# Performance work log

Hardware: AMD Instinct MI355X
Metric: run time of the kernel (lower is better)

The kernel has to match this reference:

```python
import jax, jax.numpy as jnp
import numpy as np

B = 128           # persons in batch
V = 128           # visits per person
CPV = 16          # codes per visit
MAX_VISITS = 510  # 512 - 2, hard-coded in module
D = 256           # embedding_dim * n_heads = 128 * 2
H = 2             # n_heads
DH = D // H
MAX_DAYS = 365
VOCAB = 30000
N_LAYERS = 2
DFF = 4 * D


def setup_inputs() -> dict:
    key = jax.random.key(0)
    ks = jax.random.split(key, 24)
    total_visits = B * V
    total_codes = total_visits * CPV
    all_codes = jax.random.randint(ks[0], (total_codes,), 0, VOCAB, dtype=jnp.int32)
    # code -> visit segment id (contiguous, as produced by the per-person loop)
    seg_ids = (jnp.arange(total_codes, dtype=jnp.int32) // CPV).astype(jnp.int32)
    # visit -> flattened slot in padded [B, MAX_VISITS] tensor (right-aligned)
    pos = MAX_VISITS - V + jnp.arange(V, dtype=jnp.int32)
    dest = (jnp.arange(B, dtype=jnp.int32)[:, None] * MAX_VISITS + pos[None, :]).reshape(-1)
    times = jax.random.uniform(ks[1], (total_visits,), minval=0.0, maxval=float(MAX_DAYS), dtype=jnp.float32)
    s = 0.02
    concept_emb = jax.random.normal(ks[2], (VOCAB, D), dtype=jnp.float32) * s
    pad_emb = jnp.zeros((D,), dtype=jnp.float32)
    Wq = jax.random.normal(ks[3], (N_LAYERS, D, D), dtype=jnp.float32) * s
    Wk = jax.random.normal(ks[4], (N_LAYERS, D, D), dtype=jnp.float32) * s
    Wv = jax.random.normal(ks[5], (N_LAYERS, D, D), dtype=jnp.float32) * s
    Wo = jax.random.normal(ks[6], (N_LAYERS, D, D), dtype=jnp.float32) * s
    W1 = jax.random.normal(ks[7], (N_LAYERS, D, DFF), dtype=jnp.float32) * s
    W2 = jax.random.normal(ks[8], (N_LAYERS, DFF, D), dtype=jnp.float32) * s
    z = lambda *sh: jnp.zeros(sh, dtype=jnp.float32)
    o = lambda *sh: jnp.ones(sh, dtype=jnp.float32)
    return dict(all_codes=all_codes, seg_ids=seg_ids, dest=dest, times=times,
                concept_emb=concept_emb, pad_emb=pad_emb,
                Wq=Wq, Wk=Wk, Wv=Wv, Wo=Wo,
                bq=z(N_LAYERS, D), bk=z(N_LAYERS, D), bv=z(N_LAYERS, D), bo=z(N_LAYERS, D),
                ln1_g=o(N_LAYERS, D), ln1_b=z(N_LAYERS, D),
                W1=W1, b1=z(N_LAYERS, DFF), W2=W2, b2=z(N_LAYERS, D),
                ln2_g=o(N_LAYERS, D), ln2_b=z(N_LAYERS, D))


def _ln(x, g, b):
    m = jnp.mean(x, axis=-1, keepdims=True)
    v = jnp.var(x, axis=-1, keepdims=True)
    return g * (x - m) * jax.lax.rsqrt(v + 1e-5) + b


def _forward(all_codes, seg_ids, dest, times, concept_emb, pad_emb,
             Wq, Wk, Wv, Wo, bq, bk, bv, bo, ln1_g, ln1_b,
             W1, b1, W2, b2, ln2_g, ln2_b):
    # gather code embeddings and segment-sum per visit (index_add_ in torch)
    emb = concept_emb[all_codes]                               # [total_codes, D]
    summed = jax.ops.segment_sum(emb, seg_ids, num_segments=B * V)  # [B*V, D]
    # scatter visits right-aligned into padded [B*MAX_VISITS, D], pad slots = pad_emb
    padded = jnp.broadcast_to(pad_emb, (B * MAX_VISITS, D)).at[dest].set(summed)
    # sinusoidal time embedding: timescales = ((1/1e4)**(1/D))**arange(D/2)
    t = jnp.clip(times, 0.0, float(MAX_DAYS - 1))
    ts = jnp.power(jnp.float32((1.0 / 10000.0) ** (1.0 / D)), jnp.arange(D // 2, dtype=jnp.float32))
    ang = t[:, None] * ts[None, :]                             # [B*V, D/2]
    te = jnp.concatenate([jnp.sin(ang), jnp.cos(ang)], axis=1) # [B*V, D]
    te_pad = jnp.zeros((B * MAX_VISITS, D), dtype=padded.dtype).at[dest].set(te)
    x = (padded + te_pad).reshape(B, MAX_VISITS, D)
    inv_sqrt_dh = np.float32(1.0 / np.sqrt(DH))
    for l in range(N_LAYERS):
        q = (x @ Wq[l] + bq[l]).reshape(B, MAX_VISITS, H, DH)
        k = (x @ Wk[l] + bk[l]).reshape(B, MAX_VISITS, H, DH)
        v = (x @ Wv[l] + bv[l]).reshape(B, MAX_VISITS, H, DH)
        scores = jnp.einsum('bqhd,bkhd->bhqk', q, k) * inv_sqrt_dh
        attn = jax.nn.softmax(scores, axis=-1)
        ctx = jnp.einsum('bhqk,bkhd->bqhd', attn, v).reshape(B, MAX_VISITS, D)
        x = _ln(x + ctx @ Wo[l] + bo[l], ln1_g[l], ln1_b[l])
        ff = jax.nn.relu(x @ W1[l] + b1[l]) @ W2[l] + b2[l]
        x = _ln(x + ff, ln2_g[l], ln2_b[l])
    return x


def reference(all_codes, seg_ids, dest, times, concept_emb, pad_emb,
              Wq, Wk, Wv, Wo, bq, bk, bv, bo, ln1_g, ln1_b,
              W1, b1, W2, b2, ln2_g, ln2_b):
    return _forward(all_codes, seg_ids, dest, times, concept_emb, pad_emb,
                    Wq, Wk, Wv, Wo, bq, bk, bv, bo, ln1_g, ln1_b,
                    W1, b1, W2, b2, ln2_g, ln2_b)
```

## Files before the change

### kernel.cpp

```cpp
#include <hip/hip_runtime.h>
#include <cstddef>

#define BATCH 128
#define NV 128
#define CPV 16
#define MAXV 510
#define SC 256
#define NPAD 382
#define DIM 256
#define NH 2
#define DH 128
#define NLAYERS 2
#define DFF 1024
#define MROWS (BATCH * SC)

typedef __attribute__((ext_vector_type(8))) short short8;
typedef __attribute__((ext_vector_type(4))) short short4v;
typedef __attribute__((ext_vector_type(4))) float floatx4;

__device__ __forceinline__ short f2bf(float f) {
    union { float f; unsigned u; } v; v.f = f;
    unsigned r = v.u + 0x7fffu + ((v.u >> 16) & 1u);
    return (short)(r >> 16);
}
__device__ __forceinline__ float bf2f(short s) {
    union { unsigned u; float f; } v; v.u = ((unsigned)(unsigned short)s) << 16;
    return v.f;
}

__device__ __forceinline__ void gload_lds16(const short* g, short* l) {
    __builtin_amdgcn_global_load_lds(
        (const __attribute__((address_space(1))) unsigned int*)g,
        (__attribute__((address_space(3))) unsigned int*)l,
        16, 0, 0);
}

__global__ __launch_bounds__(256) void wtrans_all(const float* __restrict__ Wq,
                                                  const float* __restrict__ Wk,
                                                  const float* __restrict__ Wv,
                                                  const float* __restrict__ Wo,
                                                  const float* __restrict__ W1,
                                                  const float* __restrict__ W2,
                                                  short* __restrict__ wqkvT,
                                                  short* __restrict__ woT,
                                                  short* __restrict__ w1T,
                                                  short* __restrict__ w2T) {
    int y = blockIdx.y;
    int l = y / 6, w = y - l * 6;
    const float* src; short* dst; int K, nsh;
    switch (w) {
        case 0:  src = Wq + (size_t)l * 65536;  dst = wqkvT + (size_t)l * 196608;           K = 256;  nsh = 8;  break;
        case 1:  src = Wk + (size_t)l * 65536;  dst = wqkvT + (size_t)l * 196608 + 65536;   K = 256;  nsh = 8;  break;
        case 2:  src = Wv + (size_t)l * 65536;  dst = wqkvT + (size_t)l * 196608 + 131072;  K = 256;  nsh = 8;  break;
        case 3:  src = Wo + (size_t)l * 65536;  dst = woT   + (size_t)l * 65536;            K = 256;  nsh = 8;  break;
        case 4:  src = W1 + (size_t)l * 262144; dst = w1T   + (size_t)l * 262144;           K = 256;  nsh = 10; break;
        default: src = W2 + (size_t)l * 262144; dst = w2T   + (size_t)l * 262144;           K = 1024; nsh = 8;  break;
    }
    int N = 1 << nsh;
    int idx = blockIdx.x * 256 + threadIdx.x;
    if (idx >= K * N) return;
    int k = idx >> nsh, n = idx & (N - 1);
    dst[(size_t)n * K + k] = f2bf(src[idx]);
}

__global__ __launch_bounds__(256) void build_x(const int* __restrict__ codes,
                                               const float* __restrict__ times,
                                               const float* __restrict__ cemb,
                                               const float* __restrict__ pemb,
                                               short* __restrict__ x) {
    int row = blockIdx.x;
    int d = threadIdx.x;
    int b = row >> 8;
    int r = row & (SC - 1);
    float val;
    if (r > 128) {
        val = 0.f;
    } else if (r == 128) {
        val = pemb[d];
    } else {
        int visit = b * NV + r;
        const int* cb = codes + visit * CPV;
        float s = 0.f;
#pragma unroll
        for (int c = 0; c < CPV; ++c)
            s += cemb[(size_t)cb[c] * DIM + d];
        float t = times[visit];
        t = fminf(fmaxf(t, 0.f), 364.f);
        int i = d & 127;
        float ang = t * expf(-0.03597789207803197f * (float)i);
        float te = (d < 128) ? sinf(ang) : cosf(ang);
        val = s + te;
    }
    x[(size_t)row * DIM + d] = f2bf(val);
}

__global__ __launch_bounds__(256) void gemm_qkv(const short* __restrict__ A,
                                                const short* __restrict__ BT,
                                                const float* __restrict__ bq,
                                                const float* __restrict__ bk,
                                                const float* __restrict__ bv,
                                                short* __restrict__ qo,
                                                short* __restrict__ ko,
                                                short* __restrict__ vo) {
    __shared__ __align__(16) short lA[2][128 * 32];
    __shared__ __align__(16) short lB[2][128 * 32];
    int tid = threadIdx.x;
    int wave = tid >> 6, lane = tid & 63;
    int l15 = lane & 15, quad = lane >> 4;
    int q8 = quad * 8;
    int m0 = blockIdx.y * 128;
    int n0 = blockIdx.x * 128;
    int sel = blockIdx.x >> 1;
    int nloc = n0 & 255;
    int wm = (wave & 1) * 64;
    int wn = (wave >> 1) * 64;

    int srow = tid >> 2;
    int skoff = (tid & 3) * 8;
    const short* ag = A + (size_t)(m0 + srow) * DIM + skoff;
    const short* bg = BT + (size_t)(n0 + srow) * DIM + skoff;
    const size_t rstep = (size_t)64 * DIM;
    int t8 = tid * 8;

    floatx4 acc[4][4];
#pragma unroll
    for (int i = 0; i < 4; ++i)
#pragma unroll
        for (int j = 0; j < 4; ++j) acc[i][j] = (floatx4){0.f, 0.f, 0.f, 0.f};

    gload_lds16(ag, lA[0] + t8);
    gload_lds16(ag + rstep, lA[0] + 2048 + t8);
    gload_lds16(bg, lB[0] + t8);
    gload_lds16(bg + rstep, lB[0] + 2048 + t8);
    __syncthreads();
    int cur = 0;
#pragma unroll
    for (int k0 = 0; k0 < 8; ++k0) {
        if (k0 < 7) {
            int kn = (k0 + 1) * 32;
            gload_lds16(ag + kn, lA[cur ^ 1] + t8);
            gload_lds16(ag + rstep + kn, lA[cur ^ 1] + 2048 + t8);
            gload_lds16(bg + kn, lB[cur ^ 1] + t8);
            gload_lds16(bg + rstep + kn, lB[cur ^ 1] + 2048 + t8);
        }
        short8 aF[4], bF[4];
#pragma unroll
        for (int t = 0; t < 4; ++t) {
            aF[t] = *(const short8*)(lA[cur] + (wm + t * 16 + l15) * 32 + q8);
            bF[t] = *(const short8*)(lB[cur] + (wn + t * 16 + l15) * 32 + q8);
        }
#pragma unroll
        for (int i = 0; i < 4; ++i)
#pragma unroll
            for (int j = 0; j < 4; ++j)
                acc[i][j] = __builtin_amdgcn_mfma_f32_16x16x32_bf16(aF[i], bF[j], acc[i][j], 0, 0, 0);
        __syncthreads();
        cur ^= 1;
    }

    const float* bias = (sel == 0) ? bq : (sel == 1) ? bk : bv;
    short* out = (sel == 0) ? qo : (sel == 1) ? ko : vo;
#pragma unroll
    for (int j = 0; j < 4; ++j) {
        int col = nloc + wn + j * 16 + l15;
        float bval = bias[col];
#pragma unroll
        for (int i = 0; i < 4; ++i) {
#pragma unroll
            for (int r = 0; r < 4; ++r) {
                int row = m0 + wm + i * 16 + quad * 4 + r;
                out[(size_t)row * DIM + col] = f2bf(acc[i][j][r] + bval);
            }
        }
    }
}

__global__ __launch_bounds__(256) void gemm_wo_ln(const short* __restrict__ CTX,
                                                  const short* __restrict__ WoT,
                                                  const float* __restrict__ bo,
                                                  const short* __restrict__ X,
                                                  const float* __restrict__ g,
                                                  const float* __restrict__ bta,
                                                  short* __restrict__ xout) {
    __shared__ __align__(16) short lA[2][64 * 32];
    __shared__ __align__(16) short lB[2][256 * 32];
    int tid = threadIdx.x;
    int wave = tid >> 6, lane = tid & 63;
    int l15 = lane & 15, quad = lane >> 4;
    int q8 = quad * 8;
    int m0 = blockIdx.x * 64;
    int wr = wave * 16;
    int srow = tid >> 2;
    int skoff = (tid & 3) * 8;
    const short* ag = CTX + (size_t)(m0 + srow) * DIM + skoff;
    const short* bg = WoT + (size_t)srow * DIM + skoff;
    int t8 = tid * 8;

    floatx4 acc[16];
#pragma unroll
    for (int j = 0; j < 16; ++j) acc[j] = (floatx4){0.f, 0.f, 0.f, 0.f};

    gload_lds16(ag, lA[0] + t8);
    gload_lds16(bg, lB[0] + t8);
    gload_lds16(bg + (size_t)64 * DIM, lB[0] + 2048 + t8);
    gload_lds16(bg + (size_t)128 * DIM, lB[0] + 4096 + t8);
    gload_lds16(bg + (size_t)192 * DIM, lB[0] + 6144 + t8);
    __syncthreads();
    int cur = 0;
#pragma unroll
    for (int k0 = 0; k0 < 8; ++k0) {
        if (k0 < 7) {
            int kn = (k0 + 1) * 32;
            gload_lds16(ag + kn, lA[cur ^ 1] + t8);
            gload_lds16(bg + kn, lB[cur ^ 1] + t8);
            gload_lds16(bg + (size_t)64 * DIM + kn, lB[cur ^ 1] + 2048 + t8);
            gload_lds16(bg + (size_t)128 * DIM + kn, lB[cur ^ 1] + 4096 + t8);
            gload_lds16(bg + (size_t)192 * DIM + kn, lB[cur ^ 1] + 6144 + t8);
        }
        short8 aF = *(const short8*)(lA[cur] + (wr + l15) * 32 + q8);
#pragma unroll
        for (int j = 0; j < 16; ++j) {
            short8 bF = *(const short8*)(lB[cur] + (j * 16 + l15) * 32 + q8);
            acc[j] = __builtin_amdgcn_mfma_f32_16x16x32_bf16(aF, bF, acc[j], 0, 0, 0);
        }
        __syncthreads();
        cur ^= 1;
    }

    float bias[16], gam[16], bet[16];
#pragma unroll
    for (int j = 0; j < 16; ++j) {
        int col = j * 16 + l15;
        bias[j] = bo[col]; gam[j] = g[col]; bet[j] = bta[col];
    }
#pragma unroll
    for (int r = 0; r < 4; ++r) {
        int row = m0 + wr + quad * 4 + r;
        float v[16], s = 0.f, sq = 0.f;
#pragma unroll
        for (int j = 0; j < 16; ++j) {
            v[j] = acc[j][r] + bias[j] + bf2f(X[(size_t)row * DIM + j * 16 + l15]);
            s += v[j]; sq += v[j] * v[j];
        }
        s += __shfl_xor(s, 1); sq += __shfl_xor(sq, 1);
        s += __shfl_xor(s, 2); sq += __shfl_xor(sq, 2);
        s += __shfl_xor(s, 4); sq += __shfl_xor(sq, 4);
        s += __shfl_xor(s, 8); sq += __shfl_xor(sq, 8);
        float mean = s * (1.f / 256.f);
        float var = fmaxf(sq * (1.f / 256.f) - mean * mean, 0.f);
        float rstd = rsqrtf(var + 1e-5f);
#pragma unroll
        for (int j = 0; j < 16; ++j) {
            float y = gam[j] * (v[j] - mean) * rstd + bet[j];
            xout[(size_t)row * DIM + j * 16 + l15] = f2bf(y);
        }
    }
}

#define PST 136
__global__ __launch_bounds__(256, 2) void ff_fused(const short* __restrict__ X,
                                                   const short* __restrict__ W1T,
                                                   const float* __restrict__ b1,
                                                   const short* __restrict__ W2T,
                                                   const float* __restrict__ b2,
                                                   const float* __restrict__ g2,
                                                   const float* __restrict__ bt2,
                                                   short* __restrict__ xout,
                                                   float* __restrict__ fout,
                                                   float* __restrict__ padrow) {
    __shared__ __align__(16) short lA[2][64 * 32];
    __shared__ __align__(16) short lB[2][128 * 32];
    __shared__ __align__(16) short lB2[2][256 * 32];
    __shared__ __align__(16) short lP[64 * PST];
    __shared__ float redS[4][32], redQ[4][32];
    int tid = threadIdx.x;
    int wave = tid >> 6, lane = tid & 63;
    int l15 = lane & 15, quad = lane >> 4;
    int q8 = quad * 8;
    int m0 = blockIdx.x * 64;
    int wm = (wave & 1) * 32;
    int wf = (wave >> 1) * 64;
    int wn2 = (wave >> 1) * 128;
    int srow = tid >> 2;
    int spart = (tid & 3) * 8;
    const short* xg = X + (size_t)(m0 + srow) * DIM + spart;
    int t8 = tid * 8;

    floatx4 acc2[2][8];
#pragma unroll
    for (int i = 0; i < 2; ++i)
#pragma unroll
        for (int j = 0; j < 8; ++j) acc2[i][j] = (floatx4){0.f, 0.f, 0.f, 0.f};

    for (int f0 = 0; f0 < DFF; f0 += 128) {
        const short* w1g = W1T + (size_t)(f0 + srow) * DIM + spart;
        floatx4 acc1[2][4];
#pragma unroll
        for (int i = 0; i < 2; ++i)
#pragma unroll
            for (int j = 0; j < 4; ++j) acc1[i][j] = (floatx4){0.f, 0.f, 0.f, 0.f};

        gload_lds16(xg, lA[0] + t8);
        gload_lds16(w1g, lB[0] + t8);
        gload_lds16(w1g + (size_t)64 * DIM, lB[0] + 2048 + t8);
        __syncthreads();
        int cur = 0;
#pragma unroll
        for (int k0 = 0; k0 < 8; ++k0) {
            if (k0 < 7) {
                int kn = (k0 + 1) * 32;
                gload_lds16(xg + kn, lA[cur ^ 1] + t8);
                gload_lds16(w1g + kn, lB[cur ^ 1] + t8);
                gload_lds16(w1g + (size_t)64 * DIM + kn, lB[cur ^ 1] + 2048 + t8);
            }
            short8 aF[2], bF[4];
#pragma unroll
            for (int t = 0; t < 2; ++t)
                aF[t] = *(const short8*)(lA[cur] + (wm + t * 16 + l15) * 32 + q8);
#pragma unroll
            for (int t = 0; t < 4; ++t)
                bF[t] = *(const short8*)(lB[cur] + (wf + t * 16 + l15) * 32 + q8);
#pragma unroll
            for (int i = 0; i < 2; ++i)
#pragma unroll
                for (int j = 0; j < 4; ++j)
                    acc1[i][j] = __builtin_amdgcn_mfma_f32_16x16x32_bf16(aF[i], bF[j], acc1[i][j], 0, 0, 0);
            __syncthreads();
            cur ^= 1;
        }

        {
            const short* w2g = W2T + (size_t)srow * DFF + f0 + spart;
            gload_lds16(w2g, lB2[0] + t8);
            gload_lds16(w2g + (size_t)64 * DFF, lB2[0] + 2048 + t8);
            gload_lds16(w2g + (size_t)128 * DFF, lB2[0] + 4096 + t8);
            gload_lds16(w2g + (size_t)192 * DFF, lB2[0] + 6144 + t8);
        }
#pragma unroll
        for (int j = 0; j < 4; ++j) {
            int fc = wf + j * 16 + l15;
            float bval = b1[f0 + fc];
#pragma unroll
            for (int i = 0; i < 2; ++i) {
#pragma unroll
                for (int r = 0; r < 4; ++r) {
                    float v = acc1[i][j][r] + bval;
                    lP[(wm + i * 16 + quad * 4 + r) * PST + fc] = f2bf(fmaxf(v, 0.f));
                }
            }
        }
        __syncthreads();
        cur = 0;
#pragma unroll
        for (int ks = 0; ks < 4; ++ks) {
            if (ks < 3) {
                const short* w2g = W2T + (size_t)srow * DFF + f0 + (ks + 1) * 32 + spart;
                gload_lds16(w2g, lB2[cur ^ 1] + t8);
                gload_lds16(w2g + (size_t)64 * DFF, lB2[cur ^ 1] + 2048 + t8);
                gload_lds16(w2g + (size_t)128 * DFF, lB2[cur ^ 1] + 4096 + t8);
                gload_lds16(w2g + (size_t)192 * DFF, lB2[cur ^ 1] + 6144 + t8);
            }
            short8 aP[2], bW[8];
#pragma unroll
            for (int t = 0; t < 2; ++t)
                aP[t] = *(const short8*)(lP + (wm + t * 16 + l15) * PST + ks * 32 + q8);
#pragma unroll
            for (int j = 0; j < 8; ++j)
                bW[j] = *(const short8*)(lB2[cur] + (wn2 + j * 16 + l15) * 32 + q8);
#pragma unroll
            for (int i = 0; i < 2; ++i)
#pragma unroll
                for (int j = 0; j < 8; ++j)
                    acc2[i][j] = __builtin_amdgcn_mfma_f32_16x16x32_bf16(aP[i], bW[j], acc2[i][j], 0, 0, 0);
            __syncthreads();
            cur ^= 1;
        }
    }

    float b2v[8];
#pragma unroll
    for (int j = 0; j < 8; ++j) b2v[j] = b2[wn2 + j * 16 + l15];
#pragma unroll
    for (int i = 0; i < 2; ++i) {
#pragma unroll
        for (int r = 0; r < 4; ++r) {
            int row = m0 + wm + i * 16 + quad * 4 + r;
            float s = 0.f, sq = 0.f;
#pragma unroll
            for (int j = 0; j < 8; ++j) {
                float v = acc2[i][j][r] + b2v[j] + bf2f(X[(size_t)row * DIM + wn2 + j * 16 + l15]);
                acc2[i][j][r] = v;
                s += v; sq += v * v;
            }
            s += __shfl_xor(s, 1); sq += __shfl_xor(sq, 1);
            s += __shfl_xor(s, 2); sq += __shfl_xor(sq, 2);
            s += __shfl_xor(s, 4); sq += __shfl_xor(sq, 4);
            s += __shfl_xor(s, 8); sq += __shfl_xor(sq, 8);
            if (l15 == 0) {
                int idx = i * 16 + quad * 4 + r;
                redS[wave][idx] = s;
                redQ[wave][idx] = sq;
            }
        }
    }
    __syncthreads();
    float gam[8], bet[8];
#pragma unroll
    for (int j = 0; j < 8; ++j) {
        int col = wn2 + j * 16 + l15;
        gam[j] = g2[col]; bet[j] = bt2[col];
    }
#pragma unroll
    for (int i = 0; i < 2; ++i) {
#pragma unroll
        for (int r = 0; r < 4; ++r) {
            int idx = i * 16 + quad * 4 + r;
            float ts = redS[wave][idx] + redS[wave ^ 2][idx];
            float tq = redQ[wave][idx] + redQ[wave ^ 2][idx];
            float mean = ts * (1.f / 256.f);
            float var = fmaxf(tq * (1.f / 256.f) - mean * mean, 0.f);
            float rstd = rsqrtf(var + 1e-5f);
            int grow = m0 + wm + i * 16 + quad * 4 + r;
            if (!fout) {
#pragma unroll
                for (int j = 0; j < 8; ++j) {
                    float y = gam[j] * (acc2[i][j][r] - mean) * rstd + bet[j];
                    xout[(size_t)grow * DIM + wn2 + j * 16 + l15] = f2bf(y);
                }
            } else {
                int b = grow >> 8, rr = grow & 255;
                if (rr < 128) {
                    float* dst = fout + ((size_t)b * MAXV + NPAD + rr) * DIM;
#pragma unroll
                    for (int j = 0; j < 8; ++j) {
                        float y = gam[j] * (acc2[i][j][r] - mean) * rstd + bet[j];
                        dst[wn2 + j * 16 + l15] = y;
                    }
                } else if (rr == 128) {
#pragma unroll
                    for (int j = 0; j < 8; ++j) {
                        float y = gam[j] * (acc2[i][j][r] - mean) * rstd + bet[j];
                        padrow[(size_t)b * DIM + wn2 + j * 16 + l15] = y;
                    }
                }
            }
        }
    }
}

__global__ __launch_bounds__(256) void pad_bcast(const float* __restrict__ padrow,
                                                 float* __restrict__ fout) {
    int b = blockIdx.y;
    int p = blockIdx.x * 4 + (threadIdx.x >> 6);
    if (p >= NPAD) return;
    int d4 = (threadIdx.x & 63) * 4;
    floatx4 v = *(const floatx4*)(padrow + (size_t)b * DIM + d4);
    *(floatx4*)(fout + ((size_t)b * MAXV + p) * DIM + d4) = v;
}

__global__ __launch_bounds__(256) void transpose_v(const short* __restrict__ v,
                                                   short* __restrict__ vT) {
    __shared__ short lds[32][33];
    int pair = blockIdx.y;
    int b = pair >> 1, h = pair & 1;
    int st = (blockIdx.x & 7) * 32;
    int dt = (blockIdx.x >> 3) * 32;
    int tid = threadIdx.x;
    int sl = tid >> 3, dl = (tid & 7) * 4;
    const short* src = v + ((size_t)(b * SC + st + sl)) * DIM + h * DH + dt + dl;
    short4v val = *(const short4v*)src;
#pragma unroll
    for (int j = 0; j < 4; ++j) lds[sl][dl + j] = val[j];
    __syncthreads();
    int drow = tid >> 3, scol = (tid & 7) * 4;
    short* dst = vT + (size_t)pair * DH * SC + (size_t)(dt + drow) * SC + st + scol;
#pragma unroll
    for (int j = 0; j < 4; ++j) dst[j] = lds[scol + j][drow];
}

#define AST 136
__global__ __launch_bounds__(256) void attn_fused(const short* __restrict__ q,
                                                  const short* __restrict__ k,
                                                  const short* __restrict__ vT,
                                                  short* __restrict__ ctx) {
    __shared__ __align__(16) short lA[128 * 32];
    __shared__ __align__(16) short lB[128 * 32];
    __shared__ __align__(16) short lS[128 * AST];
    int tid = threadIdx.x;
    int wave = tid >> 6, lane = tid & 63;
    int l15 = lane & 15, quad = lane >> 4;
    int q8 = quad * 8;
    int pair = blockIdx.y;
    int b = pair >> 1, h = pair & 1;
    int m0 = blockIdx.x * 128;
    int wm = (wave & 1) * 64;
    int wn = (wave >> 1) * 64;

    const short* Qb = q + ((size_t)b * SC) * DIM + h * DH;
    const short* Kb = k + ((size_t)b * SC) * DIM + h * DH;
    const short* Vb = vT + (size_t)pair * DH * SC;
    int srow = tid >> 2;
    int skoff = (tid & 3) * 8;
    short* lA_dst = lA + tid * 8;
    short* lB_dst = lB + tid * 8;
    const size_t rstep = (size_t)64 * DIM;
    const short* ag = Qb + (size_t)(m0 + srow) * DIM + skoff;
    const float scale = 0.08838834764831845f;

    floatx4 oacc[4][4];
#pragma unroll
    for (int i = 0; i < 4; ++i)
#pragma unroll
        for (int j = 0; j < 4; ++j) oacc[i][j] = (floatx4){0.f, 0.f, 0.f, 0.f};
    float rsum[4] = {0.f, 0.f, 0.f, 0.f};

    for (int kt = 0; kt < 2; ++kt) {
        const short* bg = Kb + (size_t)(kt * 128 + srow) * DIM + skoff;
        floatx4 sacc[4][4];
#pragma unroll
        for (int i = 0; i < 4; ++i)
#pragma unroll
            for (int j = 0; j < 4; ++j) sacc[i][j] = (floatx4){0.f, 0.f, 0.f, 0.f};
#pragma unroll
        for (int k0 = 0; k0 < DH; k0 += 32) {
            gload_lds16(ag + k0, lA_dst);
            gload_lds16(ag + rstep + k0, lA_dst + 2048);
            gload_lds16(bg + k0, lB_dst);
            gload_lds16(bg + rstep + k0, lB_dst + 2048);
            __syncthreads();
            short8 aF[4], bF[4];
#pragma unroll
            for (int t = 0; t < 4; ++t) {
                aF[t] = *(const short8*)(lA + (wm + t * 16 + l15) * 32 + q8);
                bF[t] = *(const short8*)(lB + (wn + t * 16 + l15) * 32 + q8);
            }
#pragma unroll
            for (int i = 0; i < 4; ++i)
#pragma unroll
                for (int j = 0; j < 4; ++j)
                    sacc[i][j] = __builtin_amdgcn_mfma_f32_16x16x32_bf16(aF[i], bF[j], sacc[i][j], 0, 0, 0);
            __syncthreads();
        }
#pragma unroll
        for (int j = 0; j < 4; ++j) {
            int col = wn + j * 16 + l15;
            int cg = kt * 128 + col;
            float w = (cg < 128) ? 1.f : ((cg == 128) ? (float)NPAD : 0.f);
#pragma unroll
            for (int i = 0; i < 4; ++i) {
#pragma unroll
                for (int r = 0; r < 4; ++r) {
                    float e = __expf(fminf(sacc[i][j][r] * scale, 30.f));
                    lS[(wm + i * 16 + quad * 4 + r) * AST + col] = f2bf(w * e);
                }
            }
        }
        __syncthreads();
#pragma unroll
        for (int ks = 0; ks < 4; ++ks) {
            const short* vg = Vb + (size_t)srow * SC + kt * 128 + ks * 32 + skoff;
            gload_lds16(vg, lB_dst);
            gload_lds16(vg + (size_t)64 * SC, lB_dst + 2048);
            __syncthreads();
            short8 aP[4], bV[4];
#pragma unroll
            for (int t = 0; t < 4; ++t) {
                aP[t] = *(const short8*)(lS + (wm + t * 16 + l15) * AST + ks * 32 + q8);
                bV[t] = *(const short8*)(lB + (wn + t * 16 + l15) * 32 + q8);
            }
#pragma unroll
            for (int i = 0; i < 4; ++i) {
                float s = 0.f;
#pragma unroll
                for (int e = 0; e < 8; ++e) s += bf2f(aP[i][e]);
                rsum[i] += s;
            }
#pragma unroll
            for (int i = 0; i < 4; ++i)
#pragma unroll
                for (int j = 0; j < 4; ++j)
                    oacc[i][j] = __builtin_amdgcn_mfma_f32_16x16x32_bf16(aP[i], bV[j], oacc[i][j], 0, 0, 0);
            __syncthreads();
        }
    }

#pragma unroll
    for (int i = 0; i < 4; ++i) {
        rsum[i] += __shfl_xor(rsum[i], 16);
        rsum[i] += __shfl_xor(rsum[i], 32);
    }
    short* outb = ctx + ((size_t)(b * SC + m0)) * DIM + h * DH;
#pragma unroll
    for (int i = 0; i < 4; ++i) {
#pragma unroll
        for (int r = 0; r < 4; ++r) {
            float inv = 1.f / __shfl(rsum[i], quad * 4 + r);
#pragma unroll
            for (int j = 0; j < 4; ++j) {
                int col = wn + j * 16 + l15;
                int row = wm + i * 16 + quad * 4 + r;
                outb[(size_t)row * DIM + col] = f2bf(oacc[i][j][r] * inv);
            }
        }
    }
}

extern "C" void kernel_launch(void* const* d_in, const int* in_sizes, int n_in,
                              void* d_out, int out_size, void* d_ws, size_t ws_size,
                              hipStream_t stream) {
    const int*   all_codes = (const int*)d_in[0];
    const float* times = (const float*)d_in[3];
    const float* cemb  = (const float*)d_in[4];
    const float* pemb  = (const float*)d_in[5];
    const float* Wq = (const float*)d_in[6];
    const float* Wk = (const float*)d_in[7];
    const float* Wv = (const float*)d_in[8];
    const float* Wo = (const float*)d_in[9];
    const float* bq = (const float*)d_in[10];
    const float* bk = (const float*)d_in[11];
    const float* bv = (const float*)d_in[12];
    const float* bo = (const float*)d_in[13];
    const float* ln1g = (const float*)d_in[14];
    const float* ln1b = (const float*)d_in[15];
    const float* W1 = (const float*)d_in[16];
    const float* b1 = (const float*)d_in[17];
    const float* W2 = (const float*)d_in[18];
    const float* b2 = (const float*)d_in[19];
    const float* ln2g = (const float*)d_in[20];
    const float* ln2b = (const float*)d_in[21];

    char* ws = (char*)d_ws;
    short* wqkvT = (short*)ws;
    short* woT   = wqkvT + 2 * 196608;
    short* w1T   = woT + 2 * 65536;
    short* w2T   = w1T + 2 * 262144;
    float* padrow = (float*)(ws + (3500u << 10));

    const size_t SLOT = (size_t)MROWS * DIM;
    short* xb = (short*)(ws + (4u << 20));
    short* C0 = xb + SLOT;
    short* C1 = C0 + SLOT;
    short* C2 = C1 + SLOT;
    short* C3 = C2 + SLOT;
    short* C4 = C3 + SLOT;

    wtrans_all<<<dim3(1024, 12), 256, 0, stream>>>(Wq, Wk, Wv, Wo, W1, W2,
                                                   wqkvT, woT, w1T, w2T);
    build_x<<<MROWS, 256, 0, stream>>>(all_codes, times, cemb, pemb, xb);

    for (int l = 0; l < NLAYERS; ++l) {
        const short* qkv_l = wqkvT + (size_t)l * 196608;
        const short* wo_l = woT + (size_t)l * 65536;
        const short* w1_l = w1T + (size_t)l * 262144;
        const short* w2_l = w2T + (size_t)l * 262144;
        int last = (l == NLAYERS - 1);

        gemm_qkv<<<dim3(6, MROWS / 128), 256, 0, stream>>>(xb, qkv_l, bq + l * 256, bk + l * 256,
                                                           bv + l * 256, C0, C1, C2);
        transpose_v<<<dim3(32, BATCH * NH), 256, 0, stream>>>(C2, C4);
        attn_fused<<<dim3(2, BATCH * NH), 256, 0, stream>>>(C0, C1, C4, C3);
        gemm_wo_ln<<<MROWS / 64, 256, 0, stream>>>(C3, wo_l, bo + l * 256, xb,
                                                   ln1g + l * 256, ln1b + l * 256, C0);
        ff_fused<<<MROWS / 64, 256, 0, stream>>>(C0, w1_l, b1 + l * 1024, w2_l, b2 + l * 256,
                                                 ln2g + l * 256, ln2b + l * 256, xb,
                                                 last ? (float*)d_out : nullptr,
                                                 last ? padrow : nullptr);
        if (last)
            pad_bcast<<<dim3(96, BATCH), 256, 0, stream>>>(padrow, (float*)d_out);
    }
}
```

Measured before the change: 458.7 us.

## Drop padded rows from main GEMMs and handle the pad row separately

Shrinks the per-person sequence from 256 slots (128 real visits, one pad representative, zero rows) to exactly 128 real rows. This halves the rows in the QKV, Wo and FFN GEMMs and in attention. The single shared pad row is computed by small per-batch kernels: pad_qkv projects it, and pad_tail runs its attention, Wo+LN and FFN+LN with scalar dot products. Attention appends the pad key as an extra column weighted by 382, with V transposed to a 160 stride. This adds extra launches and slow scalar per-row kernels in exchange for halving the bulk work.

```diff
diff --git a/kernel.cpp b/kernel.cpp
--- a/kernel.cpp
+++ b/kernel.cpp
@@ -5,14 +5,15 @@
 #define NV 128
 #define CPV 16
 #define MAXV 510
-#define SC 256
 #define NPAD 382
 #define DIM 256
 #define NH 2
 #define DH 128
 #define NLAYERS 2
 #define DFF 1024
-#define MROWS (BATCH * SC)
+#define MROWS (BATCH * NV)
+#define AST 168
+#define VST 160
 
 typedef __attribute__((ext_vector_type(8))) short short8;
 typedef __attribute__((ext_vector_type(4))) short short4v;
@@ -66,32 +67,28 @@
 __global__ __launch_bounds__(256) void build_x(const int* __restrict__ codes,
                                                const float* __restrict__ times,
                                                const float* __restrict__ cemb,
-                                               const float* __restrict__ pemb,
                                                short* __restrict__ x) {
     int row = blockIdx.x;
     int d = threadIdx.x;
-    int b = row >> 8;
-    int r = row & (SC - 1);
-    float val;
-    if (r > 128) {
-        val = 0.f;
-    } else if (r == 128) {
-        val = pemb[d];
-    } else {
-        int visit = b * NV + r;
-        const int* cb = codes + visit * CPV;
-        float s = 0.f;
-#pragma unroll
-        for (int c = 0; c < CPV; ++c)
-            s += cemb[(size_t)cb[c] * DIM + d];
-        float t = times[visit];
-        t = fminf(fmaxf(t, 0.f), 364.f);
-        int i = d & 127;
-        float ang = t * expf(-0.03597789207803197f * (float)i);
-        float te = (d < 128) ? sinf(ang) : cosf(ang);
-        val = s + te;
-    }
-    x[(size_t)row * DIM + d] = f2bf(val);
+    int b = row >> 7;
+    int r = row & 127;
+    int visit = b * NV + r;
+    const int* cb = codes + visit * CPV;
+    float s = 0.f;
+#pragma unroll
+    for (int c = 0; c < CPV; ++c)
+        s += cemb[(size_t)cb[c] * DIM + d];
+    float t = times[visit];
+    t = fminf(fmaxf(t, 0.f), 364.f);
+    int i = d & 127;
+    float ang = t * expf(-0.03597789207803197f * (float)i);
+    float te = (d < 128) ? sinf(ang) : cosf(ang);
+    x[(size_t)row * DIM + d] = f2bf(s + te);
+}
+
+__global__ __launch_bounds__(256) void build_xpad(const float* __restrict__ pemb,
+                                                  short* __restrict__ xpad) {
+    xpad[(size_t)blockIdx.x * DIM + threadIdx.x] = f2bf(pemb[threadIdx.x]);
 }
 
 __global__ __launch_bounds__(256) void gemm_qkv(const short* __restrict__ A,
@@ -175,6 +172,30 @@
     }
 }
 
+__global__ __launch_bounds__(256) void pad_qkv(const short* __restrict__ xpad,
+                                               const short* __restrict__ qkvT,
+                                               const float* __restrict__ bq,
+                                               const float* __restrict__ bk,
+                                               const float* __restrict__ bv,
+                                               float* __restrict__ padQ,
+                                               short* __restrict__ padK,
+                                               short* __restrict__ padV) {
+    __shared__ float x[256];
+    int b = blockIdx.x, tid = threadIdx.x;
+    x[tid] = bf2f(xpad[(size_t)b * DIM + tid]);
+    __syncthreads();
+#pragma unroll
+    for (int w = 0; w < 3; ++w) {
+        const short* wr = qkvT + (size_t)w * 65536 + (size_t)tid * 256;
+        float a = 0.f;
+#pragma unroll 8
+        for (int k = 0; k < 256; ++k) a += x[k] * bf2f(wr[k]);
+        if (w == 0)      padQ[(size_t)b * DIM + tid] = a + bq[tid];
+        else if (w == 1) padK[(size_t)b * DIM + tid] = f2bf(a + bk[tid]);
+        else             padV[(size_t)b * DIM + tid] = f2bf(a + bv[tid]);
+    }
+}
+
 __global__ __launch_bounds__(256) void gemm_wo_ln(const short* __restrict__ CTX,
                                                   const short* __restrict__ WoT,
                                                   const float* __restrict__ bo,
@@ -266,8 +287,7 @@
                                                    const float* __restrict__ g2,
                                                    const float* __restrict__ bt2,
                                                    short* __restrict__ xout,
-                                                   float* __restrict__ fout,
-                                                   float* __restrict__ padrow) {
+                                                   float* __restrict__ fout) {
     __shared__ __align__(16) short lA[2][64 * 32];
     __shared__ __align__(16) short lB[2][128 * 32];
     __shared__ __align__(16) short lB2[2][256 * 32];
@@ -428,23 +448,127 @@
                     xout[(size_t)grow * DIM + wn2 + j * 16 + l15] = f2bf(y);
                 }
             } else {
-                int b = grow >> 8, rr = grow & 255;
-                if (rr < 128) {
-                    float* dst = fout + ((size_t)b * MAXV + NPAD + rr) * DIM;
-#pragma unroll
-                    for (int j = 0; j < 8; ++j) {
-                        float y = gam[j] * (acc2[i][j][r] - mean) * rstd + bet[j];
-                        dst[wn2 + j * 16 + l15] = y;
-                    }
-                } else if (rr == 128) {
-#pragma unroll
-                    for (int j = 0; j < 8; ++j) {
-                        float y = gam[j] * (acc2[i][j][r] - mean) * rstd + bet[j];
-                        padrow[(size_t)b * DIM + wn2 + j * 16 + l15] = y;
-                    }
+                int bb = grow >> 7, rr = grow & 127;
+                float* dst = fout + ((size_t)bb * MAXV + NPAD + rr) * DIM;
+#pragma unroll
+                for (int j = 0; j < 8; ++j) {
+                    float y = gam[j] * (acc2[i][j][r] - mean) * rstd + bet[j];
+                    dst[wn2 + j * 16 + l15] = y;
                 }
             }
         }
+    }
+}
+
+__global__ __launch_bounds__(256) void pad_tail(const float* __restrict__ padQ,
+                                                const short* __restrict__ padK,
+                                                const short* __restrict__ padV,
+                                                const short* __restrict__ kmain,
+                                                const short* __restrict__ vmain,
+                                                const short* __restrict__ woT,
+                                                const float* __restrict__ bo,
+                                                const float* __restrict__ g1,
+                                                const float* __restrict__ bt1,
+                                                const short* __restrict__ w1T,
+                                                const float* __restrict__ b1,
+                                                const short* __restrict__ w2T,
+                                                const float* __restrict__ b2,
+                                                const float* __restrict__ g2,
+                                                const float* __restrict__ bt2,
+                                                short* __restrict__ xpad,
+                                                float* __restrict__ padrowF) {
+    __shared__ float qv[256], wgt[2][128], wp[2], den[2], ctx[256], h1[256], ff[1024];
+    __shared__ float red[4][2];
+    int b = blockIdx.x, tid = threadIdx.x;
+    int wave = tid >> 6, lane = tid & 63;
+    const float scale = 0.08838834764831845f;
+
+    qv[tid] = padQ[(size_t)b * DIM + tid];
+    __syncthreads();
+    int h = tid >> 7, kk = tid & 127;
+    {
+        const short* krow = kmain + (size_t)(b * NV + kk) * DIM + h * DH;
+        float s = 0.f;
+#pragma unroll 8
+        for (int d = 0; d < DH; ++d) s += bf2f(krow[d]) * qv[h * DH + d];
+        wgt[h][kk] = __expf(fminf(s * scale, 30.f));
+    }
+    if (kk == 0) {
+        const short* kp = padK + (size_t)b * DIM + h * DH;
+        float sp = 0.f;
+#pragma unroll 8
+        for (int d = 0; d < DH; ++d) sp += bf2f(kp[d]) * qv[h * DH + d];
+        wp[h] = 382.f * __expf(fminf(sp * scale, 30.f));
+    }
+    __syncthreads();
+    if (kk == 0) {
+        float dsum = wp[h];
+        for (int i = 0; i < 128; ++i) dsum += wgt[h][i];
+        den[h] = dsum;
+    }
+    __syncthreads();
+    {
+        const short* vcol = vmain + (size_t)(b * NV) * DIM + h * DH + kk;
+        float c = 0.f;
+#pragma unroll 8
+        for (int key = 0; key < 128; ++key) c += wgt[h][key] * bf2f(vcol[(size_t)key * DIM]);
+        c += wp[h] * bf2f(padV[(size_t)b * DIM + h * DH + kk]);
+        ctx[h * DH + kk] = c / den[h];
+    }
+    __syncthreads();
+    float t;
+    {
+        const short* wr = woT + (size_t)tid * 256;
+        float a = 0.f;
+#pragma unroll 8
+        for (int k = 0; k < 256; ++k) a += ctx[k] * bf2f(wr[k]);
+        t = a + bo[tid] + bf2f(xpad[(size_t)b * DIM + tid]);
+    }
+    {
+        float s = t, sq = t * t;
+#pragma unroll
+        for (int off = 1; off < 64; off <<= 1) { s += __shfl_xor(s, off); sq += __shfl_xor(sq, off); }
+        if (lane == 0) { red[wave][0] = s; red[wave][1] = sq; }
+        __syncthreads();
+        float ts = red[0][0] + red[1][0] + red[2][0] + red[3][0];
+        float tq = red[0][1] + red[1][1] + red[2][1] + red[3][1];
+        float mean = ts * (1.f / 256.f);
+        float var = fmaxf(tq * (1.f / 256.f) - mean * mean, 0.f);
+        float rstd = rsqrtf(var + 1e-5f);
+        h1[tid] = g1[tid] * (t - mean) * rstd + bt1[tid];
+    }
+    __syncthreads();
+#pragma unroll
+    for (int u = 0; u < 4; ++u) {
+        int f = u * 256 + tid;
+        const short* wr = w1T + (size_t)f * 256;
+        float a = 0.f;
+#pragma unroll 8
+        for (int k = 0; k < 256; ++k) a += h1[k] * bf2f(wr[k]);
+        ff[f] = fmaxf(a + b1[f], 0.f);
+    }
+    __syncthreads();
+    {
+        const short* wr = w2T + (size_t)tid * DFF;
+        float a = 0.f;
+#pragma unroll 8
+        for (int f = 0; f < DFF; ++f) a += ff[f] * bf2f(wr[f]);
+        t = a + b2[tid] + h1[tid];
+    }
+    {
+        float s = t, sq = t * t;
+#pragma unroll
+        for (int off = 1; off < 64; off <<= 1) { s += __shfl_xor(s, off); sq += __shfl_xor(sq, off); }
+        if (lane == 0) { red[wave][0] = s; red[wave][1] = sq; }
+        __syncthreads();
+        float ts = red[0][0] + red[1][0] + red[2][0] + red[3][0];
+        float tq = red[0][1] + red[1][1] + red[2][1] + red[3][1];
+        float mean = ts * (1.f / 256.f);
+        float var = fmaxf(tq * (1.f / 256.f) - mean * mean, 0.f);
+        float rstd = rsqrtf(var + 1e-5f);
+        float y = g2[tid] * (t - mean) * rstd + bt2[tid];
+        xpad[(size_t)b * DIM + tid] = f2bf(y);
+        if (padrowF) padrowF[(size_t)b * DIM + tid] = y;
     }
 }
 
@@ -459,139 +583,167 @@
 }
 
 __global__ __launch_bounds__(256) void transpose_v(const short* __restrict__ v,
+                                                   const short* __restrict__ padV,
                                                    short* __restrict__ vT) {
     __shared__ short lds[32][33];
     int pair = blockIdx.y;
     int b = pair >> 1, h = pair & 1;
-    int st = (blockIdx.x & 7) * 32;
-    int dt = (blockIdx.x >> 3) * 32;
+    int st = blockIdx.x % 5;
+    int dt = blockIdx.x / 5;
     int tid = threadIdx.x;
     int sl = tid >> 3, dl = (tid & 7) * 4;
-    const short* src = v + ((size_t)(b * SC + st + sl)) * DIM + h * DH + dt + dl;
-    short4v val = *(const short4v*)src;
+    short4v val;
+    if (st < 4) {
+        const short* src = v + ((size_t)(b * NV + st * 32 + sl)) * DIM + h * DH + dt * 32 + dl;
+        val = *(const short4v*)src;
+    } else {
+        val = (short4v){0, 0, 0, 0};
+        if (sl == 0)
+            val = *(const short4v*)(padV + (size_t)b * DIM + h * DH + dt * 32 + dl);
+    }
 #pragma unroll
     for (int j = 0; j < 4; ++j) lds[sl][dl + j] = val[j];
     __syncthreads();
     int drow = tid >> 3, scol = (tid & 7) * 4;
-    short* dst = vT + (size_t)pair * DH * SC + (size_t)(dt + drow) * SC + st + scol;
+    short* dst = vT + (size_t)pair * DH * VST + (size_t)(dt * 32 + drow) * VST + st * 32 + scol;
 #pragma unroll
     for (int j = 0; j < 4; ++j) dst[j] = lds[scol + j][drow];
 }
 
-#define AST 136
 __global__ __launch_bounds__(256) void attn_fused(const short* __restrict__ q,
                                                   const short* __restrict__ k,
                                                   const short* __restrict__ vT,
+                                                  const short* __restrict__ padK,
                                                   short* __restrict__ ctx) {
-    __shared__ __align__(16) short lA[128 * 32];
+    __shared__ __align__(16) short lA[64 * 32];
     __shared__ __align__(16) short lB[128 * 32];
-    __shared__ __align__(16) short lS[128 * AST];
+    __shared__ __align__(16) short lS[64 * AST];
     int tid = threadIdx.x;
     int wave = tid >> 6, lane = tid & 63;
     int l15 = lane & 15, quad = lane >> 4;
     int q8 = quad * 8;
     int pair = blockIdx.y;
     int b = pair >> 1, h = pair & 1;
-    int m0 = blockIdx.x * 128;
-    int wm = (wave & 1) * 64;
+    int m0 = blockIdx.x * 64;
+    int wm = (wave & 1) * 32;
     int wn = (wave >> 1) * 64;
 
-    const short* Qb = q + ((size_t)b * SC) * DIM + h * DH;
-    const short* Kb = k + ((size_t)b * SC) * DIM + h * DH;
-    const short* Vb = vT + (size_t)pair * DH * SC;
     int srow = tid >> 2;
     int skoff = (tid & 3) * 8;
+    const short* ag = q + (size_t)(b * NV + m0 + srow) * DIM + h * DH + skoff;
+    const short* bg = k + (size_t)(b * NV + srow) * DIM + h * DH + skoff;
+    const short* kp = padK + (size_t)b * DIM + h * DH + q8;
     short* lA_dst = lA + tid * 8;
     short* lB_dst = lB + tid * 8;
-    const size_t rstep = (size_t)64 * DIM;
-    const short* ag = Qb + (size_t)(m0 + srow) * DIM + skoff;
     const float scale = 0.08838834764831845f;
 
-    floatx4 oacc[4][4];
-#pragma unroll
-    for (int i = 0; i < 4; ++i)
+    {
+        int zr = tid >> 2, zc = 144 + (tid & 3) * 4;
+        *(short4v*)(lS + zr * AST + zc) = (short4v){0, 0, 0, 0};
+    }
+
+    floatx4 sacc[2][4];
+    floatx4 sacct[2];
+#pragma unroll
+    for (int i = 0; i < 2; ++i) {
+#pragma unroll
+        for (int j = 0; j < 4; ++j) sacc[i][j] = (floatx4){0.f, 0.f, 0.f, 0.f};
+        sacct[i] = (floatx4){0.f, 0.f, 0.f, 0.f};
+    }
+
+#pragma unroll
+    for (int k0 = 0; k0 < DH; k0 += 32) {
+        gload_lds16(ag + k0, lA_dst);
+        gload_lds16(bg + k0, lB_dst);
+        gload_lds16(bg + (size_t)64 * DIM + k0, lB_dst + 2048);
+        __syncthreads();
+        short8 aF[2], bF[4];
+#pragma unroll
+        for (int t = 0; t < 2; ++t)
+            aF[t] = *(const short8*)(lA + (wm + t * 16 + l15) * 32 + q8);
+#pragma unroll
+        for (int t = 0; t < 4; ++t)
+            bF[t] = *(const short8*)(lB + (wn + t * 16 + l15) * 32 + q8);
+#pragma unroll
+        for (int i = 0; i < 2; ++i)
+#pragma unroll
+            for (int j = 0; j < 4; ++j)
+                sacc[i][j] = __builtin_amdgcn_mfma_f32_16x16x32_bf16(aF[i], bF[j], sacc[i][j], 0, 0, 0);
+        if (wn == 0) {
+            short8 bFt = (l15 == 0) ? *(const short8*)(kp + k0) : (short8){0,0,0,0,0,0,0,0};
+#pragma unroll
+            for (int i = 0; i < 2; ++i)
+                sacct[i] = __builtin_amdgcn_mfma_f32_16x16x32_bf16(aF[i], bFt, sacct[i], 0, 0, 0);
+        }
+        __syncthreads();
+    }
+#pragma unroll
+    for (int j = 0; j < 4; ++j) {
+        int col = wn + j * 16 + l15;
+#pragma unroll
+        for (int i = 0; i < 2; ++i) {
+#pragma unroll
+            for (int r = 0; r < 4; ++r) {
+                lS[(wm + i * 16 + quad * 4 + r) * AST + col] =
+                    f2bf(__expf(fminf(sacc[i][j][r] * scale, 30.f)));
+            }
+        }
+    }
+    if (wn == 0) {
+        float wt = (l15 == 0) ? 382.f : 0.f;
+#pragma unroll
+        for (int i = 0; i < 2; ++i) {
+#pragma unroll
+            for (int r = 0; r < 4; ++r) {
+                lS[(wm + i * 16 + quad * 4 + r) * AST + 128 + l15] =
+                    f2bf(wt * __expf(fminf(sacct[i][r] * scale, 30.f)));
+            }
+        }
+    }
+    __syncthreads();
+    const short* vg = vT + (size_t)pair * DH * VST + (size_t)srow * VST + skoff;
+    floatx4 oacc[2][4];
+#pragma unroll
+    for (int i = 0; i < 2; ++i)
 #pragma unroll
         for (int j = 0; j < 4; ++j) oacc[i][j] = (floatx4){0.f, 0.f, 0.f, 0.f};
-    float rsum[4] = {0.f, 0.f, 0.f, 0.f};
-
-    for (int kt = 0; kt < 2; ++kt) {
-        const short* bg = Kb + (size_t)(kt * 128 + srow) * DIM + skoff;
-        floatx4 sacc[4][4];
-#pragma unroll
-        for (int i = 0; i < 4; ++i)
-#pragma unroll
-            for (int j = 0; j < 4; ++j) sacc[i][j] = (floatx4){0.f, 0.f, 0.f, 0.f};
-#pragma unroll
-        for (int k0 = 0; k0 < DH; k0 += 32) {
-            gload_lds16(ag + k0, lA_dst);
-            gload_lds16(ag + rstep + k0, lA_dst + 2048);
-            gload_lds16(bg + k0, lB_dst);
-            gload_lds16(bg + rstep + k0, lB_dst + 2048);
-            __syncthreads();
-            short8 aF[4], bF[4];
-#pragma unroll
-            for (int t = 0; t < 4; ++t) {
-                aF[t] = *(const short8*)(lA + (wm + t * 16 + l15) * 32 + q8);
-                bF[t] = *(const short8*)(lB + (wn + t * 16 + l15) * 32 + q8);
-            }
-#pragma unroll
-            for (int i = 0; i < 4; ++i)
-#pragma unroll
-                for (int j = 0; j < 4; ++j)
-                    sacc[i][j] = __builtin_amdgcn_mfma_f32_16x16x32_bf16(aF[i], bF[j], sacc[i][j], 0, 0, 0);
-            __syncthreads();
-        }
-#pragma unroll
-        for (int j = 0; j < 4; ++j) {
-            int col = wn + j * 16 + l15;
-            int cg = kt * 128 + col;
-            float w = (cg < 128) ? 1.f : ((cg == 128) ? (float)NPAD : 0.f);
-#pragma unroll
-            for (int i = 0; i < 4; ++i) {
-#pragma unroll
-                for (int r = 0; r < 4; ++r) {
-                    float e = __expf(fminf(sacc[i][j][r] * scale, 30.f));
-                    lS[(wm + i * 16 + quad * 4 + r) * AST + col] = f2bf(w * e);
-                }
-            }
-        }
-        __syncthreads();
-#pragma unroll
-        for (int ks = 0; ks < 4; ++ks) {
-            const short* vg = Vb + (size_t)srow * SC + kt * 128 + ks * 32 + skoff;
-            gload_lds16(vg, lB_dst);
-            gload_lds16(vg + (size_t)64 * SC, lB_dst + 2048);
-            __syncthreads();
-            short8 aP[4], bV[4];
-#pragma unroll
-            for (int t = 0; t < 4; ++t) {
-                aP[t] = *(const short8*)(lS + (wm + t * 16 + l15) * AST + ks * 32 + q8);
-                bV[t] = *(const short8*)(lB + (wn + t * 16 + l15) * 32 + q8);
-            }
-#pragma unroll
-            for (int i = 0; i < 4; ++i) {
-                float s = 0.f;
-#pragma unroll
-                for (int e = 0; e < 8; ++e) s += bf2f(aP[i][e]);
-                rsum[i] += s;
-            }
-#pragma unroll
-            for (int i = 0; i < 4; ++i)
-#pragma unroll
-                for (int j = 0; j < 4; ++j)
-                    oacc[i][j] = __builtin_amdgcn_mfma_f32_16x16x32_bf16(aP[i], bV[j], oacc[i][j], 0, 0, 0);
-            __syncthreads();
-        }
-    }
-
-#pragma unroll
-    for (int i = 0; i < 4; ++i) {
+    float rsum[2] = {0.f, 0.f};
+
+#pragma unroll
+    for (int ks = 0; ks < 5; ++ks) {
+        gload_lds16(vg + ks * 32, lB_dst);
+        gload_lds16(vg + (size_t)64 * VST + ks * 32, lB_dst + 2048);
+        __syncthreads();
+        short8 aP[2], bV[4];
+#pragma unroll
+        for (int t = 0; t < 2; ++t)
+            aP[t] = *(const short8*)(lS + (wm + t * 16 + l15) * AST + ks * 32 + q8);
+#pragma unroll
+        for (int t = 0; t < 4; ++t)
+            bV[t] = *(const short8*)(lB + (wn + t * 16 + l15) * 32 + q8);
+#pragma unroll
+        for (int i = 0; i < 2; ++i) {
+            float s = 0.f;
+#pragma unroll
+            for (int e = 0; e < 8; ++e) s += bf2f(aP[i][e]);
+            rsum[i] += s;
+        }
+#pragma unroll
+        for (int i = 0; i < 2; ++i)
+#pragma unroll
+            for (int j = 0; j < 4; ++j)
+                oacc[i][j] = __builtin_amdgcn_mfma_f32_16x16x32_bf16(aP[i], bV[j], oacc[i][j], 0, 0, 0);
+        __syncthreads();
+    }
+
+#pragma unroll
+    for (int i = 0; i < 2; ++i) {
         rsum[i] += __shfl_xor(rsum[i], 16);
         rsum[i] += __shfl_xor(rsum[i], 32);
     }
-    short* outb = ctx + ((size_t)(b * SC + m0)) * DIM + h * DH;
-#pragma unroll
-    for (int i = 0; i < 4; ++i) {
+    short* outb = ctx + (size_t)(b * NV + m0) * DIM + h * DH;
+#pragma unroll
+    for (int i = 0; i < 2; ++i) {
 #pragma unroll
         for (int r = 0; r < 4; ++r) {
             float inv = 1.f / __shfl(rsum[i], quad * 4 + r);
@@ -634,7 +786,13 @@
     short* woT   = wqkvT + 2 * 196608;
     short* w1T   = woT + 2 * 65536;
     short* w2T   = w1T + 2 * 262144;
-    float* padrow = (float*)(ws + (3500u << 10));
+
+    char* aux = ws + (3400u << 10);
+    float* padQ   = (float*)aux;
+    short* padK   = (short*)(aux + 131072);
+    short* padV   = padK + 32768;
+    short* xpad   = padV + 32768;
+    float* padrowF = (float*)(aux + 131072 + 3 * 65536);
 
     const size_t SLOT = (size_t)MROWS * DIM;
     short* xb = (short*)(ws + (4u << 20));
@@ -646,7 +804,8 @@
 
     wtrans_all<<<dim3(1024, 12), 256, 0, stream>>>(Wq, Wk, Wv, Wo, W1, W2,
                                                    wqkvT, woT, w1T, w2T);
-    build_x<<<MROWS, 256, 0, stream>>>(all_codes, times, cemb, pemb, xb);
+    build_x<<<MROWS, 256, 0, stream>>>(all_codes, times, cemb, xb);
+    build_xpad<<<BATCH, 256, 0, stream>>>(pemb, xpad);
 
     for (int l = 0; l < NLAYERS; ++l) {
         const short* qkv_l = wqkvT + (size_t)l * 196608;
@@ -657,15 +816,21 @@
 
         gemm_qkv<<<dim3(6, MROWS / 128), 256, 0, stream>>>(xb, qkv_l, bq + l * 256, bk + l * 256,
                                                            bv + l * 256, C0, C1, C2);
-        transpose_v<<<dim3(32, BATCH * NH), 256, 0, stream>>>(C2, C4);
-        attn_fused<<<dim3(2, BATCH * NH), 256, 0, stream>>>(C0, C1, C4, C3);
+        pad_qkv<<<BATCH, 256, 0, stream>>>(xpad, qkv_l, bq + l * 256, bk + l * 256,
+                                           bv + l * 256, padQ, padK, padV);
+        transpose_v<<<dim3(20, BATCH * NH), 256, 0, stream>>>(C2, padV, C4);
+        attn_fused<<<dim3(2, BATCH * NH), 256, 0, stream>>>(C0, C1, C4, padK, C3);
         gemm_wo_ln<<<MROWS / 64, 256, 0, stream>>>(C3, wo_l, bo + l * 256, xb,
                                                    ln1g + l * 256, ln1b + l * 256, C0);
         ff_fused<<<MROWS / 64, 256, 0, stream>>>(C0, w1_l, b1 + l * 1024, w2_l, b2 + l * 256,
                                                  ln2g + l * 256, ln2b + l * 256, xb,
-                                                 last ? (float*)d_out : nullptr,
-                                                 last ? padrow : nullptr);
+                                                 last ? (float*)d_out : nullptr);
+        pad_tail<<<BATCH, 256, 0, stream>>>(padQ, padK, padV, C1, C2,
+                                            wo_l, bo + l * 256, ln1g + l * 256, ln1b + l * 256,
+                                            w1_l, b1 + l * 1024, w2_l, b2 + l * 256,
+                                            ln2g + l * 256, ln2b + l * 256,
+                                            xpad, last ? padrowF : nullptr);
         if (last)
-            pad_bcast<<<dim3(96, BATCH), 256, 0, stream>>>(padrow, (float*)d_out);
-    }
-}
+            pad_bcast<<<dim3(96, BATCH), 256, 0, stream>>>(padrowF, (float*)d_out);
+    }
+}
```

New measurement: 539.7 us. 17.7% more time.
